# Kernel optimization log

Hardware: AMD Instinct MI355X
Metric: run time of the kernel (lower is better)

## Reference

```python
import jax, jax.numpy as jnp
import numpy as np

B, CIN, H, W = 64, 3, 96, 96
COUT, KH, KW = 96, 5, 5
STRIDE, PAD = 2, 2
LR, K_TOP, DELTA, P_LEB = 0.02, 2, -0.4, 3.0
PREC = 1e-30


def im2col(x):
    # torch nn.Unfold ordering: channel-major (C, kh, kw) flattened -> [B, C*KH*KW, L]
    xp = jnp.pad(x, ((0, 0), (0, 0), (PAD, PAD), (PAD, PAD)))
    Hout = (H + 2 * PAD - KH) // STRIDE + 1
    Wout = (W + 2 * PAD - KW) // STRIDE + 1
    cols = []
    for i in range(KH):  # small fixed kernel loop (25 slices)
        for j in range(KW):
            cols.append(xp[:, :, i:i + STRIDE * (Hout - 1) + 1:STRIDE,
                           j:j + STRIDE * (Wout - 1) + 1:STRIDE])
    patches = jnp.stack(cols, axis=2)  # [B, C, KH*KW, Hout, Wout]
    return patches.reshape(x.shape[0], CIN * KH * KW, Hout * Wout)  # [B, K, L]


def setup_inputs() -> dict:
    key = jax.random.key(0)
    k1, k2 = jax.random.split(key)
    inp = jax.random.normal(k1, (B, CIN, H, W), dtype=jnp.float32)
    weight = jax.random.normal(k2, (COUT, CIN, KH, KW), dtype=jnp.float32)  # init.normal_
    return {"input": inp, "weight": weight}


def reference(input, weight):
    # standard conv forward (F.conv2d, no bias)
    out = jax.lax.conv_general_dilated(
        input, weight, (STRIDE, STRIDE), [(PAD, PAD), (PAD, PAD)],
        dimension_numbers=("NCHW", "OIHW", "NCHW"))

    # --- Krotov-Hopfield Hebbian update ---
    pre = im2col(input)                      # [B, K, L]
    Wm = weight.reshape(COUT, -1)            # [O, K]
    # sign(W) * |W|^(p-1) @ pre
    tot = jnp.einsum("ok,bkl->bol", jnp.sign(Wm) * jnp.abs(Wm) ** (P_LEB - 1.0), pre)  # [B,O,L]

    Bn, _, L = tot.shape
    _, idx = jax.lax.top_k(tot.transpose(0, 2, 1), K_TOP)   # [B, L, k] over output channels
    vals = jnp.concatenate([jnp.ones((1,), tot.dtype),
                            jnp.full((K_TOP - 1,), DELTA, tot.dtype)])  # top-1 -> 1.0, rest -> delta
    act = jnp.zeros((Bn, L, COUT), tot.dtype).at[
        jnp.arange(Bn)[:, None, None], jnp.arange(L)[None, :, None], idx
    ].set(jnp.broadcast_to(vals, (Bn, L, K_TOP)))
    act = act.transpose(0, 2, 1)             # [B, O, L]

    yx = jnp.einsum("bol,bkl->ok", act, pre) / L          # mean over L, sum over batch
    yy = (act * tot).sum(0).mean(1)                        # [O]
    ds = yx - yy[:, None] * Wm                             # [O, K]
    nc = jnp.maximum(jnp.max(jnp.abs(ds)), PREC)
    new_weight = weight + LR * (ds / nc).reshape(weight.shape)
    return out, new_weight
```

## Files before the change

kernel.cpp:

```cpp
#include <hip/hip_runtime.h>

#define B_     64
#define HW_    96
#define COUT_  96
#define KK_    75
#define KPAD   96
#define HOUT_  48
#define L_     2304
#define LR_    0.02f
#define DELTA_ -0.4f
#define OUT_ELEMS (B_*COUT_*L_)
#define XPITCH 100
#define XSLOTS 3368
#define C2     192
#define NPART  (B_*12)
#define ROW    (COUT_*KK_ + COUT_)
#define X2P    99
#define X2N    (33*X2P)
#define CTP    196

typedef __attribute__((ext_vector_type(8))) short short8v;
typedef __attribute__((ext_vector_type(4))) float float4v;
typedef __attribute__((ext_vector_type(4))) unsigned uint4v;

__device__ __forceinline__ unsigned short f2bf(float f) {
  unsigned u = __float_as_uint(f);
  u += 0x7fff + ((u >> 16) & 1);
  return (unsigned short)(u >> 16);
}

__device__ __forceinline__ void ins2(float v, int o, float& v1, int& o1,
                                     float& v2, int& o2) {
  bool b1 = (v > v1) || (v == v1 && o < o1);
  bool b2 = (v > v2) || (v == v2 && o < o2);
  if (b1)      { v2 = v1; o2 = o1; v1 = v; o1 = o; }
  else if (b2) { v2 = v;  o2 = o; }
}

__global__ __launch_bounds__(256) void k0_prep(const float* __restrict__ w,
                                               unsigned short* __restrict__ wbf) {
  int i = blockIdx.x * 256 + threadIdx.x;
  if (i >= 192 * KPAD) return;
  int row = i / KPAD, k = i - row * KPAD;
  float v = 0.0f;
  if (k < KK_) {
    float ww = w[(row % COUT_) * KK_ + k];
    v = (row < COUT_) ? ww : ww * fabsf(ww);
  }
  wbf[i] = f2bf(v);
}

__device__ __forceinline__ int wswz(int blk, int row) {
  return (blk < 8) ? (blk ^ (row & 7)) : (blk ^ (row & 3));
}

__global__ __launch_bounds__(256, 3) void k1_mfma(
    const float* __restrict__ x, const unsigned short* __restrict__ wbf,
    float* __restrict__ out, float4* __restrict__ top2)
{
  __shared__ __align__(16) char ldsRaw[50336];
  unsigned short* wlds = (unsigned short*)ldsRaw;
  float* xs = (float*)(ldsRaw + 36864);
  float* cT = xs;
  const int tid = threadIdx.x;
  const int lane = tid & 63, wq = tid >> 6;
  const int b = blockIdx.y;
  const int bx = blockIdx.x;
  const int col = lane & 15, g = lane >> 4;
  const float* xb = x + (size_t)b * (3 * HW_ * HW_);

  #pragma unroll
  for (int i = 0; i < 9; ++i) {
    int id = tid + i * 256;
    int row = id / 12, blk = id - row * 12;
    uint4v v = *(const uint4v*)(wbf + row * KPAD + blk * 8);
    *(uint4v*)((char*)wlds + row * 192 + wswz(blk, row) * 16) = v;
  }

  const int ihbase = 8 * bx - 2;
  #pragma unroll
  for (int i = 0; i < 14; ++i) {
    int idx = tid + i * 256;
    if (idx < XSLOTS) {
      int row = idx / XPITCH, iwr = idx - row * XPITCH;
      int c = row / 11, ihr = row - c * 11;
      int ih = ihbase + ihr, iw = iwr - 2;
      float v = 0.0f;
      if (c < 3 && (unsigned)ih < (unsigned)HW_ && (unsigned)iw < (unsigned)HW_)
        v = xb[(c * HW_ + ih) * HW_ + iw];
      xs[idx] = v;
    }
  }

  int offs[12][2];
  {
    const int base_fl = wq * 200 + 2 * col;
    #pragma unroll
    for (int kt = 0; kt < 3; ++kt)
      #pragma unroll
      for (int e2 = 0; e2 < 4; ++e2)
        #pragma unroll
        for (int par = 0; par < 2; ++par) {
          int k = kt * 32 + g * 8 + 2 * e2 + par;
          int c = k / 25, r = k - 25 * c, ki = r / 5, kj = r - 5 * ki;
          int fl = (k < KK_) ? base_fl + (c * 11 + ki) * XPITCH + kj
                             : 33 * XPITCH;
          offs[kt * 4 + e2][par] = fl * 4;
        }
  }

  __syncthreads();

  short8v bfr[3][3];
  #pragma unroll
  for (int nt = 0; nt < 3; ++nt)
    #pragma unroll
    for (int kt = 0; kt < 3; ++kt) {
      uint4v pk;
      #pragma unroll
      for (int e2 = 0; e2 < 4; ++e2) {
        const float* p0 = (const float*)((const char*)xs + offs[kt*4+e2][0]);
        const float* p1 = (const float*)((const char*)xs + offs[kt*4+e2][1]);
        float v0 = p0[nt * 32];
        float v1 = p1[nt * 32];
        pk[e2] = (unsigned)f2bf(v0) | ((unsigned)f2bf(v1) << 16);
      }
      bfr[nt][kt] = __builtin_bit_cast(short8v, pk);
    }

  const int lrow0 = (4 * bx + wq) * 48;

  {
    float4v acc[3][6];
    #pragma unroll
    for (int nt = 0; nt < 3; ++nt)
      #pragma unroll
      for (int mt = 0; mt < 6; ++mt) acc[nt][mt] = (float4v)(0.0f);
    #pragma unroll
    for (int kt = 0; kt < 3; ++kt) {
      const int blk = kt * 4 + g;
      #pragma unroll
      for (int mt = 0; mt < 6; ++mt) {
        const int row = 96 + mt * 16 + col;
        short8v afr = *(const short8v*)(
            (const char*)wlds + row * 192 + wswz(blk, row) * 16);
        #pragma unroll
        for (int nt = 0; nt < 3; ++nt)
          acc[nt][mt] = __builtin_amdgcn_mfma_f32_16x16x32_bf16(
              afr, bfr[nt][kt], acc[nt][mt], 0, 0, 0);
      }
    }
    #pragma unroll
    for (int nt = 0; nt < 3; ++nt) {
      float v1 = -3.0e38f, v2 = -3.0e38f;
      int o1 = 0x7fffffff, o2 = 0x7fffffff;
      #pragma unroll
      for (int mt = 0; mt < 6; ++mt)
        #pragma unroll
        for (int r = 0; r < 4; ++r)
          ins2(acc[nt][mt][r], mt * 16 + g * 4 + r, v1, o1, v2, o2);
      #pragma unroll
      for (int st = 0; st < 2; ++st) {
        const int d = (st == 0) ? 16 : 32;
        float bv1 = __shfl_xor(v1, d, 64);
        int   bo1 = __shfl_xor(o1, d, 64);
        float bv2 = __shfl_xor(v2, d, 64);
        int   bo2 = __shfl_xor(o2, d, 64);
        ins2(bv1, bo1, v1, o1, v2, o2);
        ins2(bv2, bo2, v1, o1, v2, o2);
      }
      if (g == 0)
        top2[(size_t)b * L_ + lrow0 + nt * 16 + col] =
            make_float4(v1, __int_as_float(o1), v2, __int_as_float(o2));
    }
  }

  __syncthreads();

  const int blockl = bx * 192;
  #pragma unroll 1
  for (int mt = 0; mt < 6; ++mt) {
    float4v a0 = (float4v)(0.0f), a1 = (float4v)(0.0f), a2 = (float4v)(0.0f);
    #pragma unroll
    for (int kt = 0; kt < 3; ++kt) {
      const int blk = kt * 4 + g;
      const int row = mt * 16 + col;
      short8v afr = *(const short8v*)(
          (const char*)wlds + row * 192 + wswz(blk, row) * 16);
      a0 = __builtin_amdgcn_mfma_f32_16x16x32_bf16(afr, bfr[0][kt], a0, 0, 0, 0);
      a1 = __builtin_amdgcn_mfma_f32_16x16x32_bf16(afr, bfr[1][kt], a1, 0, 0, 0);
      a2 = __builtin_amdgcn_mfma_f32_16x16x32_bf16(afr, bfr[2][kt], a2, 0, 0, 0);
    }
    #pragma unroll
    for (int r = 0; r < 4; ++r) {
      const int chl = g * 4 + r;
      float* cp = cT + chl * CTP + wq * 48 + col;
      cp[0]  = a0[r];
      cp[16] = a1[r];
      cp[32] = a2[r];
    }
    __syncthreads();
    const float4* cT4 = (const float4*)cT;
    #pragma unroll
    for (int i = 0; i < 3; ++i) {
      int idx = tid + i * 256;
      int ch = idx / 48, p4 = idx - ch * 48;
      float4 v = cT4[ch * (CTP / 4) + p4];
      *(float4*)&out[((size_t)b * COUT_ + mt * 16 + ch) * L_ + blockl + 4 * p4] = v;
    }
    if (mt < 5) __syncthreads();
  }
}

__global__ __launch_bounds__(256, 2) void k2_gemm(
    const float* __restrict__ x, const float4* __restrict__ top2,
    float* __restrict__ part)
{
  __shared__ __align__(16) unsigned short actS[COUT_ * C2];
  __shared__ __align__(16) unsigned short preT[COUT_ * C2];
  __shared__ __align__(16) unsigned short xsb[X2N + 13];
  __shared__ float yyS[COUT_];
  const int tid = threadIdx.x;
  const int b = blockIdx.y;
  const int bx = blockIdx.x;
  const int l0 = bx * C2;
  const float* xb = x + (size_t)b * (3 * HW_ * HW_);

  {
    float4* a4 = (float4*)actS;
    #pragma unroll
    for (int i = 0; i < 9; ++i) a4[tid + i * 256] = make_float4(0, 0, 0, 0);
    float4* p4 = (float4*)((char*)preT + KK_ * (C2 * 2));
    if (tid < 252) {
      p4[2 * tid]     = make_float4(0, 0, 0, 0);
      p4[2 * tid + 1] = make_float4(0, 0, 0, 0);
    }
    if (tid < COUT_) yyS[tid] = 0.0f;
  }

  const int ihb2 = 8 * bx - 2;
  #pragma unroll
  for (int i = 0; i < 13; ++i) {
    int idx = tid + i * 256;
    if (idx < X2N) {
      int row = idx / X2P, iwr = idx - row * X2P;
      int c = row / 11, ihr = row - c * 11;
      int ih = ihb2 + ihr, iw = iwr - 2;
      float v = 0.0f;
      if (c < 3 && (unsigned)ih < (unsigned)HW_ && (unsigned)iw < (unsigned)HW_)
        v = xb[(c * HW_ + ih) * HW_ + iw];
      xsb[idx] = f2bf(v);
    }
  }
  __syncthreads();

  if (tid < C2) {
    const int pos = tid;
    const int ohr = pos / HOUT_, ow = pos - ohr * HOUT_;
    const int pblk = pos >> 3, plo = (pos & 7) << 1;
    const unsigned short* xl = xsb + (2 * ohr) * X2P + 2 * ow;
    #pragma unroll
    for (int c = 0; c < 3; ++c)
      #pragma unroll
      for (int ki = 0; ki < 5; ++ki)
        #pragma unroll
        for (int kj = 0; kj < 5; ++kj) {
          int k = c * 25 + ki * 5 + kj;
          unsigned short v = xl[(c * 11 + ki) * X2P + kj];
          *(unsigned short*)((char*)preT +
              k * (C2 * 2) + ((pblk ^ (k & 7)) << 4) + plo) = v;
        }
    float4 t2 = top2[(size_t)b * L_ + l0 + pos];
    int o1 = __float_as_int(t2.y), o2 = __float_as_int(t2.w);
    *(unsigned short*)((char*)actS +
        o1 * (C2 * 2) + ((pblk ^ (o1 & 7)) << 4) + plo) = 0x3F80;
    *(unsigned short*)((char*)actS +
        o2 * (C2 * 2) + ((pblk ^ (o2 & 7)) << 4) + plo) = f2bf(DELTA_);
    atomicAdd(&yyS[o1], t2.x);
    atomicAdd(&yyS[o2], DELTA_ * t2.z);
  }
  __syncthreads();

  const int lane = tid & 63, w = tid >> 6;
  const int col = lane & 15, g = lane >> 4;
  const int mb = (w >> 1) * 48, nb = (w & 1) * 48;

  float4v acc[3][3];
  #pragma unroll
  for (int mt = 0; mt < 3; ++mt)
    #pragma unroll
    for (int nt = 0; nt < 3; ++nt) acc[mt][nt] = (float4v)(0.0f);

  #pragma unroll
  for (int kt = 0; kt < 6; ++kt) {
    short8v a[3], bf[3];
    #pragma unroll
    for (int mt = 0; mt < 3; ++mt) {
      int row = mb + mt * 16 + col;
      a[mt] = *(const short8v*)((char*)actS + row * (C2 * 2) +
                                (((kt * 4 + g) ^ (row & 7)) << 4));
    }
    #pragma unroll
    for (int nt = 0; nt < 3; ++nt) {
      int row = nb + nt * 16 + col;
      bf[nt] = *(const short8v*)((char*)preT + row * (C2 * 2) +
                                 (((kt * 4 + g) ^ (row & 7)) << 4));
    }
    #pragma unroll
    for (int mt = 0; mt < 3; ++mt)
      #pragma unroll
      for (int nt = 0; nt < 3; ++nt)
        acc[mt][nt] = __builtin_amdgcn_mfma_f32_16x16x32_bf16(
            a[mt], bf[nt], acc[mt][nt], 0, 0, 0);
  }
  __syncthreads();

  float* prow = part + (size_t)(b * 12 + bx) * ROW;
  #pragma unroll
  for (int mt = 0; mt < 3; ++mt)
    #pragma unroll
    for (int nt = 0; nt < 3; ++nt)
      #pragma unroll
      for (int r = 0; r < 4; ++r) {
        int m = mb + mt * 16 + g * 4 + r;
        int n = nb + nt * 16 + col;
        if (n < KK_) prow[m * KK_ + n] = acc[mt][nt][r];
      }
  if (tid < COUT_) prow[COUT_ * KK_ + tid] = yyS[tid];
}

__global__ __launch_bounds__(256) void k3a_reduce(
    const float* __restrict__ part, float* __restrict__ tmp)
{
  __shared__ float red[4][64];
  const int e = blockIdx.x * 64 + (threadIdx.x & 63);
  const int seg = threadIdx.x >> 6;
  const int p0 = blockIdx.y * 96 + seg * 24;
  float s = 0.0f;
  #pragma unroll 4
  for (int j = 0; j < 24; ++j) s += part[(size_t)(p0 + j) * ROW + e];
  red[seg][threadIdx.x & 63] = s;
  __syncthreads();
  if (seg == 0) {
    int ll = threadIdx.x & 63;
    tmp[(size_t)blockIdx.y * ROW + e] =
        (red[0][ll] + red[1][ll]) + (red[2][ll] + red[3][ll]);
  }
}

__global__ __launch_bounds__(256) void k4_finalize(
    const float* __restrict__ w, const float* __restrict__ tmp,
    float* __restrict__ outw)
{
  __shared__ float dsS[COUT_ * KK_];
  __shared__ float yyF[COUT_];
  __shared__ float wmax[4];
  __shared__ float ncS;
  const int tid = threadIdx.x;
  if (tid < COUT_) {
    float s = 0.0f;
    #pragma unroll
    for (int p = 0; p < 8; ++p) s += tmp[(size_t)p * ROW + COUT_ * KK_ + tid];
    yyF[tid] = s;
  }
  __syncthreads();
  float m = 0.0f;
  for (int i = tid; i < COUT_ * KK_; i += 256) {
    int o = i / KK_;
    float yx = 0.0f;
    #pragma unroll
    for (int p = 0; p < 8; ++p) yx += tmp[(size_t)p * ROW + i];
    float d = yx - yyF[o] * w[i];
    dsS[i] = d;
    m = fmaxf(m, fabsf(d));
  }
  #pragma unroll
  for (int s = 32; s > 0; s >>= 1) m = fmaxf(m, __shfl_xor(m, s, 64));
  if ((tid & 63) == 0) wmax[tid >> 6] = m;
  __syncthreads();
  if (tid == 0) {
    float n = fmaxf(fmaxf(wmax[0], wmax[1]), fmaxf(wmax[2], wmax[3]));
    ncS = fmaxf(n, 1e-30f);
  }
  __syncthreads();
  const float scale = LR_ / ncS;
  for (int i = tid; i < COUT_ * KK_; i += 256) {
    outw[i] = w[i] + scale * dsS[i];
  }
}

extern "C" void kernel_launch(void* const* d_in, const int* in_sizes, int n_in,
                              void* d_out, int out_size, void* d_ws, size_t ws_size,
                              hipStream_t stream) {
  (void)in_sizes; (void)n_in; (void)out_size; (void)ws_size;
  const float* x = (const float*)d_in[0];
  const float* w = (const float*)d_in[1];
  float* out  = (float*)d_out;
  float* outw = out + OUT_ELEMS;

  unsigned short* wbf = (unsigned short*)d_ws;
  float4* top2 = (float4*)((char*)d_ws + 192 * KPAD * 2);
  float*  part = (float*)((char*)top2 + (size_t)B_ * L_ * sizeof(float4));
  float*  tmp    = part + (size_t)NPART * ROW;

  k0_prep   <<<dim3((192 * KPAD + 255) / 256), 256, 0, stream>>>(w, wbf);
  k1_mfma   <<<dim3(12, B_), 256, 0, stream>>>(x, wbf, out, top2);
  k2_gemm   <<<dim3(12, B_), 256, 0, stream>>>(x, top2, part);
  k3a_reduce<<<dim3(114, 8), 256, 0, stream>>>(part, tmp);
  k4_finalize<<<dim3(1), 256, 0, stream>>>(w, tmp, outw);
}
```

Before: 112.3 us.

## Shrink LDS footprint and register use to raise occupancy of conv MFMA kernel

The main kernel now stages the input tile in LDS as bf16 instead of fp32 and keeps only the scoring weight half in LDS. The conv-weight A fragments are read straight from global memory (L2) instead of LDS. Packed 16-bit offsets and a two-pass split of the top-2 scoring accumulators cut register pressure, and launch bounds go from 3 to 4 blocks per CU. The goal is higher occupancy and latency hiding. The cost is extra global loads in the output loop and a serialized two-half scoring loop.

```diff
diff --git a/kernel.cpp b/kernel.cpp
--- a/kernel.cpp
+++ b/kernel.cpp
@@ -11,7 +11,7 @@
 #define DELTA_ -0.4f
 #define OUT_ELEMS (B_*COUT_*L_)
 #define XPITCH 100
-#define XSLOTS 3368
+#define XSBN   3368
 #define C2     192
 #define NPART  (B_*12)
 #define ROW    (COUT_*KK_ + COUT_)
@@ -54,14 +54,14 @@
   return (blk < 8) ? (blk ^ (row & 7)) : (blk ^ (row & 3));
 }
 
-__global__ __launch_bounds__(256, 3) void k1_mfma(
+__global__ __launch_bounds__(256, 4) void k1_mfma(
     const float* __restrict__ x, const unsigned short* __restrict__ wbf,
     float* __restrict__ out, float4* __restrict__ top2)
 {
-  __shared__ __align__(16) char ldsRaw[50336];
-  unsigned short* wlds = (unsigned short*)ldsRaw;
-  float* xs = (float*)(ldsRaw + 36864);
-  float* cT = xs;
+  __shared__ __align__(16) char ldsRaw[25168];
+  unsigned short* wldsT = (unsigned short*)ldsRaw;
+  unsigned short* xsb = (unsigned short*)(ldsRaw + 18432);
+  float* cT = (float*)ldsRaw;
   const int tid = threadIdx.x;
   const int lane = tid & 63, wq = tid >> 6;
   const int b = blockIdx.y;
@@ -70,43 +70,50 @@
   const float* xb = x + (size_t)b * (3 * HW_ * HW_);
 
   #pragma unroll
-  for (int i = 0; i < 9; ++i) {
+  for (int i = 0; i < 5; ++i) {
     int id = tid + i * 256;
-    int row = id / 12, blk = id - row * 12;
-    uint4v v = *(const uint4v*)(wbf + row * KPAD + blk * 8);
-    *(uint4v*)((char*)wlds + row * 192 + wswz(blk, row) * 16) = v;
+    if (id < 1152) {
+      int row = id / 12, blk = id - row * 12;
+      uint4v v = *(const uint4v*)(wbf + (96 + row) * KPAD + blk * 8);
+      *(uint4v*)((char*)wldsT + row * 192 + wswz(blk, row) * 16) = v;
+    }
   }
 
   const int ihbase = 8 * bx - 2;
   #pragma unroll
   for (int i = 0; i < 14; ++i) {
     int idx = tid + i * 256;
-    if (idx < XSLOTS) {
-      int row = idx / XPITCH, iwr = idx - row * XPITCH;
-      int c = row / 11, ihr = row - c * 11;
-      int ih = ihbase + ihr, iw = iwr - 2;
+    if (idx < XSBN) {
       float v = 0.0f;
-      if (c < 3 && (unsigned)ih < (unsigned)HW_ && (unsigned)iw < (unsigned)HW_)
-        v = xb[(c * HW_ + ih) * HW_ + iw];
-      xs[idx] = v;
-    }
-  }
-
-  int offs[12][2];
+      if (idx < 3300) {
+        int row = idx / XPITCH, iwr = idx - row * XPITCH;
+        int c = row / 11, ihr = row - c * 11;
+        int ih = ihbase + ihr, iw = iwr - 2;
+        if ((unsigned)ih < (unsigned)HW_ && (unsigned)iw < (unsigned)HW_)
+          v = xb[(c * HW_ + ih) * HW_ + iw];
+      }
+      xsb[idx] = f2bf(v);
+    }
+  }
+
+  unsigned offsPk[12];
   {
     const int base_fl = wq * 200 + 2 * col;
     #pragma unroll
     for (int kt = 0; kt < 3; ++kt)
       #pragma unroll
-      for (int e2 = 0; e2 < 4; ++e2)
+      for (int e2 = 0; e2 < 4; ++e2) {
+        unsigned po[2];
         #pragma unroll
         for (int par = 0; par < 2; ++par) {
           int k = kt * 32 + g * 8 + 2 * e2 + par;
           int c = k / 25, r = k - 25 * c, ki = r / 5, kj = r - 5 * ki;
           int fl = (k < KK_) ? base_fl + (c * 11 + ki) * XPITCH + kj
-                             : 33 * XPITCH;
-          offs[kt * 4 + e2][par] = fl * 4;
+                             : 3300;
+          po[par] = (unsigned)(fl * 2);
         }
+        offsPk[kt * 4 + e2] = po[0] | (po[1] << 16);
+      }
   }
 
   __syncthreads();
@@ -119,31 +126,39 @@
       uint4v pk;
       #pragma unroll
       for (int e2 = 0; e2 < 4; ++e2) {
-        const float* p0 = (const float*)((const char*)xs + offs[kt*4+e2][0]);
-        const float* p1 = (const float*)((const char*)xs + offs[kt*4+e2][1]);
-        float v0 = p0[nt * 32];
-        float v1 = p1[nt * 32];
-        pk[e2] = (unsigned)f2bf(v0) | ((unsigned)f2bf(v1) << 16);
+        unsigned o = offsPk[kt * 4 + e2];
+        unsigned v0 = *(const unsigned short*)(
+            (const char*)xsb + (o & 0xffffu) + nt * 64);
+        unsigned v1 = *(const unsigned short*)(
+            (const char*)xsb + (o >> 16) + nt * 64);
+        pk[e2] = v0 | (v1 << 16);
       }
       bfr[nt][kt] = __builtin_bit_cast(short8v, pk);
     }
 
   const int lrow0 = (4 * bx + wq) * 48;
 
-  {
-    float4v acc[3][6];
+  float tv1[3], tv2[3]; int to1[3], to2[3];
+  #pragma unroll
+  for (int nt = 0; nt < 3; ++nt) {
+    tv1[nt] = -3.0e38f; tv2[nt] = -3.0e38f;
+    to1[nt] = 0x7fffffff; to2[nt] = 0x7fffffff;
+  }
+  #pragma unroll 1
+  for (int half = 0; half < 2; ++half) {
+    float4v acc[3][3];
     #pragma unroll
     for (int nt = 0; nt < 3; ++nt)
       #pragma unroll
-      for (int mt = 0; mt < 6; ++mt) acc[nt][mt] = (float4v)(0.0f);
+      for (int mt = 0; mt < 3; ++mt) acc[nt][mt] = (float4v)(0.0f);
     #pragma unroll
     for (int kt = 0; kt < 3; ++kt) {
       const int blk = kt * 4 + g;
       #pragma unroll
-      for (int mt = 0; mt < 6; ++mt) {
-        const int row = 96 + mt * 16 + col;
+      for (int mt = 0; mt < 3; ++mt) {
+        const int row = half * 48 + mt * 16 + col;
         short8v afr = *(const short8v*)(
-            (const char*)wlds + row * 192 + wswz(blk, row) * 16);
+            (const char*)wldsT + row * 192 + wswz(blk, row) * 16);
         #pragma unroll
         for (int nt = 0; nt < 3; ++nt)
           acc[nt][mt] = __builtin_amdgcn_mfma_f32_16x16x32_bf16(
@@ -151,28 +166,30 @@
       }
     }
     #pragma unroll
-    for (int nt = 0; nt < 3; ++nt) {
-      float v1 = -3.0e38f, v2 = -3.0e38f;
-      int o1 = 0x7fffffff, o2 = 0x7fffffff;
-      #pragma unroll
-      for (int mt = 0; mt < 6; ++mt)
+    for (int nt = 0; nt < 3; ++nt)
+      #pragma unroll
+      for (int mt = 0; mt < 3; ++mt)
         #pragma unroll
         for (int r = 0; r < 4; ++r)
-          ins2(acc[nt][mt][r], mt * 16 + g * 4 + r, v1, o1, v2, o2);
-      #pragma unroll
-      for (int st = 0; st < 2; ++st) {
-        const int d = (st == 0) ? 16 : 32;
-        float bv1 = __shfl_xor(v1, d, 64);
-        int   bo1 = __shfl_xor(o1, d, 64);
-        float bv2 = __shfl_xor(v2, d, 64);
-        int   bo2 = __shfl_xor(o2, d, 64);
-        ins2(bv1, bo1, v1, o1, v2, o2);
-        ins2(bv2, bo2, v1, o1, v2, o2);
-      }
-      if (g == 0)
-        top2[(size_t)b * L_ + lrow0 + nt * 16 + col] =
-            make_float4(v1, __int_as_float(o1), v2, __int_as_float(o2));
-    }
+          ins2(acc[nt][mt][r], half * 48 + mt * 16 + g * 4 + r,
+               tv1[nt], to1[nt], tv2[nt], to2[nt]);
+  }
+  #pragma unroll
+  for (int nt = 0; nt < 3; ++nt) {
+    #pragma unroll
+    for (int st = 0; st < 2; ++st) {
+      const int d = (st == 0) ? 16 : 32;
+      float bv1 = __shfl_xor(tv1[nt], d, 64);
+      int   bo1 = __shfl_xor(to1[nt], d, 64);
+      float bv2 = __shfl_xor(tv2[nt], d, 64);
+      int   bo2 = __shfl_xor(to2[nt], d, 64);
+      ins2(bv1, bo1, tv1[nt], to1[nt], tv2[nt], to2[nt]);
+      ins2(bv2, bo2, tv1[nt], to1[nt], tv2[nt], to2[nt]);
+    }
+    if (g == 0)
+      top2[(size_t)b * L_ + lrow0 + nt * 16 + col] =
+          make_float4(tv1[nt], __int_as_float(to1[nt]),
+                      tv2[nt], __int_as_float(to2[nt]));
   }
 
   __syncthreads();
@@ -183,10 +200,8 @@
     float4v a0 = (float4v)(0.0f), a1 = (float4v)(0.0f), a2 = (float4v)(0.0f);
     #pragma unroll
     for (int kt = 0; kt < 3; ++kt) {
-      const int blk = kt * 4 + g;
-      const int row = mt * 16 + col;
       short8v afr = *(const short8v*)(
-          (const char*)wlds + row * 192 + wswz(blk, row) * 16);
+          wbf + (mt * 16 + col) * KPAD + kt * 32 + g * 8);
       a0 = __builtin_amdgcn_mfma_f32_16x16x32_bf16(afr, bfr[0][kt], a0, 0, 0, 0);
       a1 = __builtin_amdgcn_mfma_f32_16x16x32_bf16(afr, bfr[1][kt], a1, 0, 0, 0);
       a2 = __builtin_amdgcn_mfma_f32_16x16x32_bf16(afr, bfr[2][kt], a2, 0, 0, 0);
```

New measurement: 118.6 us. 5.6% more time.
